# Optimization experiments

Measured on AMD Instinct MI355X. Metric: run time of the kernel, lower is better.

## Reference

```python
import jax, jax.numpy as jnp
import numpy as np

D_MODEL = 768
N_HEADS = 12
D_KEYS = 64
D_LLM = 4096
D_INNER = N_HEADS * D_KEYS  # 768


def setup_inputs() -> dict:
    key = jax.random.key(0)
    ks = jax.random.split(key, 12)
    inp = {
        "target_embedding": jax.random.normal(ks[0], (8, 1024, D_MODEL), dtype=jnp.float32),
        "source_embedding": jax.random.normal(ks[1], (1000, D_LLM), dtype=jnp.float32),
        "value_embedding": jax.random.normal(ks[2], (1000, D_LLM), dtype=jnp.float32),
        # Linear params stored as [in, out] (y = x @ W + b)
        "Wq": jax.random.normal(ks[3], (D_MODEL, D_INNER), dtype=jnp.float32) * 0.02,
        "bq": jnp.zeros((D_INNER,), dtype=jnp.float32),
        "Wk": jax.random.normal(ks[4], (D_LLM, D_INNER), dtype=jnp.float32) * 0.02,
        "bk": jnp.zeros((D_INNER,), dtype=jnp.float32),
        "Wv": jax.random.normal(ks[5], (D_LLM, D_INNER), dtype=jnp.float32) * 0.02,
        "bv": jnp.zeros((D_INNER,), dtype=jnp.float32),
        "Wo": jax.random.normal(ks[6], (D_INNER, D_LLM), dtype=jnp.float32) * 0.02,
        "bo": jnp.zeros((D_LLM,), dtype=jnp.float32),
    }
    return inp


def reference(target_embedding, source_embedding, value_embedding,
              Wq, bq, Wk, bk, Wv, bv, Wo, bo):
    B, L, _ = target_embedding.shape
    S, _ = source_embedding.shape
    H, E = N_HEADS, D_KEYS
    # projections
    q = (target_embedding @ Wq + bq).reshape(B, L, H, E)  # [B,L,H,E]
    k = (source_embedding @ Wk + bk).reshape(S, H, E)     # [S,H,E] broadcast over batch
    v = (value_embedding @ Wv + bv).reshape(S, H, E)      # [S,H,E]
    scale = 1.0 / np.sqrt(E).astype(np.float32)
    scores = jnp.einsum('blhe,she->bhls', q, k) * scale   # [B,H,L,S]
    A = jax.nn.softmax(scores, axis=-1)                   # dropout is identity at eval
    out = jnp.einsum('bhls,she->blhe', A, v).reshape(B, L, H * E)
    return out @ Wo + bo                                  # [B,L,d_llm]
```

## Files before the change

kernel.cpp:

```cpp
#include <hip/hip_runtime.h>
#include <cstdint>
#include <type_traits>


typedef unsigned short u16;
typedef __attribute__((ext_vector_type(8))) short bf16x8;
typedef __attribute__((ext_vector_type(4))) float f32x4;
typedef __attribute__((ext_vector_type(16))) float f32x16;
typedef __attribute__((ext_vector_type(4))) float fvec4;
typedef __attribute__((ext_vector_type(4))) unsigned short u16x4;
typedef __attribute__((ext_vector_type(4))) unsigned int u32x4;
typedef __attribute__((ext_vector_type(2))) unsigned int u32x2;

using gld_src_t = const __attribute__((address_space(1))) void*;
using gld_dst_t = __attribute__((address_space(3))) void*;

static __device__ __forceinline__ u16 bf16_rne(float f) {
  uint32_t u = __builtin_bit_cast(uint32_t, f);
  u += 0x7fffu + ((u >> 16) & 1u);
  return (u16)(u >> 16);
}

static __device__ __forceinline__ float exp2_fast(float x) {
  float r; asm("v_exp_f32 %0, %1" : "=v"(r) : "v"(x)); return r;
}

static __device__ __forceinline__ uint32_t pk_bf16(float a, float b) {
  return (uint32_t)bf16_rne(a) | ((uint32_t)bf16_rne(b) << 16);
}

__global__ void convert_pad_bf16(const float* __restrict__ in, u16* __restrict__ out,
                                 int validR, int C, long n4) {
  long stride = (long)gridDim.x * blockDim.x;
  for (long i = (long)blockIdx.x * blockDim.x + threadIdx.x; i < n4; i += stride) {
    long e = i << 2;
    int r = (int)(e / C);
    u16x4 o;
    if (r < validR) {
      fvec4 v = *(const fvec4*)(in + e);
      o[0] = bf16_rne(v[0]); o[1] = bf16_rne(v[1]);
      o[2] = bf16_rne(v[2]); o[3] = bf16_rne(v[3]);
    } else {
      o[0] = 0; o[1] = 0; o[2] = 0; o[3] = 0;
    }
    *(u16x4*)(out + e) = o;
  }
}

template <bool F32IN>
__global__ void transpose_to_bf16(const void* __restrict__ inv, u16* __restrict__ out,
                                  int R, int C) {
  __shared__ u16 tile[32][33];
  int bc = blockIdx.x * 32, br = blockIdx.y * 32;
  int tx = threadIdx.x & 31, ty = threadIdx.x >> 5;
#pragma unroll
  for (int i = 0; i < 4; ++i) {
    int r = br + ty + i * 8, c = bc + tx;
    u16 bits = 0;
    if (r < R && c < C) {
      if constexpr (F32IN) bits = bf16_rne(((const float*)inv)[(size_t)r * C + c]);
      else                 bits = ((const u16*)inv)[(size_t)r * C + c];
    }
    tile[ty + i * 8][tx] = bits;
  }
  __syncthreads();
#pragma unroll
  for (int i = 0; i < 4; ++i) {
    int orow = bc + ty + i * 8, oc = br + tx;
    if (orow < C && oc < R) out[(size_t)orow * R + oc] = tile[tx][ty + i * 8];
  }
}

template <typename CT>
__global__ __launch_bounds__(256, 2) void gemm_bt_128p(
    const u16* __restrict__ A, const u16* __restrict__ B,
    const float* __restrict__ bias, CT* __restrict__ C,
    int N, int K, float escale) {
  __shared__ u16 As[2][128 * 64];
  __shared__ u16 Bs[2][128 * 64];

  const int tid = threadIdx.x, lane = tid & 63, w = tid >> 6;
  const int lr = lane & 15, lg = lane >> 4;
  const int wr = (w >> 1) * 64, wc = (w & 1) * 64;

  const int nbx = N >> 7;
  const int bid = blockIdx.y * gridDim.x + blockIdx.x;
  const int cpx = (gridDim.x * gridDim.y) >> 3;
  const int swz = (bid & 7) * cpx + (bid >> 3);
  const int bm = (swz / nbx) * 128, bn = (swz % nbx) * 128;

  f32x4 acc[4][4] = {};

  auto STAGE = [&](int t, int buf) {
#pragma unroll
    for (int it = 0; it < 4; ++it) {
      const int s = it * 256 + tid;
      const int r = s >> 3;
      const int cg = (s & 7) ^ (r & 7);
      const int ldsb = (it * 256 + w * 64) * 16;
      __builtin_amdgcn_global_load_lds(
          (gld_src_t)(const void*)(A + (size_t)(bm + r) * K + t * 64 + cg * 8),
          (gld_dst_t)((char*)&As[buf][0] + ldsb), 16, 0, 0);
      __builtin_amdgcn_global_load_lds(
          (gld_src_t)(const void*)(B + (size_t)(bn + r) * K + t * 64 + cg * 8),
          (gld_dst_t)((char*)&Bs[buf][0] + ldsb), 16, 0, 0);
    }
  };

  auto LDF = [&](const u16* base, int R, int CB) {
    return *(const bf16x8*)((const char*)base + (size_t)R * 128 + (CB ^ ((R & 7) << 4)));
  };

  STAGE(0, 0);

  const int nk = K >> 6;
  for (int t = 0; t < nk; ++t) {
    const int cur = t & 1;
    if (t + 1 < nk) {
      STAGE(t + 1, cur ^ 1);
      asm volatile("s_waitcnt vmcnt(8)" ::: "memory");
    } else {
      asm volatile("s_waitcnt vmcnt(0)" ::: "memory");
    }
    __builtin_amdgcn_s_barrier();
    __builtin_amdgcn_sched_barrier(0);

    const u16* as = &As[cur][0];
    const u16* bs = &Bs[cur][0];

    bf16x8 af[4][2], bfr[4][2];
#pragma unroll
    for (int m = 0; m < 4; ++m)
#pragma unroll
      for (int kk = 0; kk < 2; ++kk)
        af[m][kk] = LDF(as, wr + m * 16 + lr, kk * 64 + lg * 16);
#pragma unroll
    for (int n = 0; n < 4; ++n)
#pragma unroll
      for (int kk = 0; kk < 2; ++kk)
        bfr[n][kk] = LDF(bs, wc + n * 16 + lr, kk * 64 + lg * 16);

    __builtin_amdgcn_s_setprio(1);
#pragma unroll
    for (int kk = 0; kk < 2; ++kk)
#pragma unroll
      for (int m = 0; m < 4; ++m)
#pragma unroll
        for (int n = 0; n < 4; ++n)
          acc[m][n] = __builtin_amdgcn_mfma_f32_16x16x32_bf16(
              af[m][kk], bfr[n][kk], acc[m][n], 0, 0, 0);
    __builtin_amdgcn_s_setprio(0);

    __builtin_amdgcn_sched_barrier(0);
    __builtin_amdgcn_s_barrier();
  }

#pragma unroll
  for (int n = 0; n < 4; ++n) {
    const int col = bn + wc + n * 16 + lr;
    const float bv = bias[col];
#pragma unroll
    for (int m = 0; m < 4; ++m) {
      const int row0 = bm + wr + m * 16 + lg * 4;
#pragma unroll
      for (int r = 0; r < 4; ++r) {
        float v = (acc[m][n][r] + bv) * escale;
        if constexpr (std::is_same<CT, u16>::value)
          C[(size_t)(row0 + r) * N + col] = bf16_rne(v);
        else
          C[(size_t)(row0 + r) * N + col] = v;
      }
    }
  }
}

__global__ __launch_bounds__(512, 2) void gemm_bt_256p(
    const u16* __restrict__ A, const u16* __restrict__ B,
    const float* __restrict__ bias, float* __restrict__ C,
    int N, int K) {
  __shared__ u16 As[4][128 * 64];
  __shared__ u16 Bs[4][128 * 64];

  const int tid = threadIdx.x, lane = tid & 63, w = tid >> 6;
  const int lr = lane & 15, lg = lane >> 4;
  const int wr = w >> 2, wcol = w & 3;

  const int nbx = N >> 8;
  const int bid = blockIdx.y * gridDim.x + blockIdx.x;
  const int cpx = (gridDim.x * gridDim.y) >> 3;
  const int swz = (bid & 7) * cpx + (bid >> 3);
  const int bm = (swz / nbx) * 256, bn = (swz % nbx) * 256;

  f32x4 acc[8][4] = {};

  auto STAGE_UNIT = [&](int t, int buf, int mat) {
#pragma unroll
    for (int it = 0; it < 2; ++it) {
      const int s = it * 512 + tid;
      const int rp = s >> 3;
      const int cl = (s & 7) ^ (rp & 7);
      const int gr = (cl >> 2) * 128 + rp;
      const int gc = cl & 3;
      const int ldsb = (it * 512 + w * 64) * 16;
      const u16* src = (mat ? B : A) + (size_t)((mat ? bn : bm) + gr) * K + t * 32 + gc * 8;
      __builtin_amdgcn_global_load_lds((gld_src_t)(const void*)src,
          (gld_dst_t)((char*)(mat ? &Bs[buf][0] : &As[buf][0]) + ldsb), 16, 0, 0);
    }
  };

  auto LDF = [&](const u16* base, int gr, int klg) {
    const int byte = (gr & 127) * 128 + (((((gr >> 7) * 4 + klg) << 4)) ^ ((gr & 7) << 4));
    return *(const bf16x8*)((const char*)base + byte);
  };

  STAGE_UNIT(0, 0, 0); STAGE_UNIT(0, 0, 1);
  STAGE_UNIT(1, 1, 0); STAGE_UNIT(1, 1, 1);
  asm volatile("s_waitcnt vmcnt(4)" ::: "memory");
  __builtin_amdgcn_s_barrier();
  __builtin_amdgcn_sched_barrier(0);

  const int nk = K >> 5;
  bf16x8 bfr[4];
  for (int t = 0; t < nk; ++t) {
    const int cur = t & 3;
    const u16* as = &As[cur][0];
    const u16* bs = &Bs[cur][0];
#pragma unroll
    for (int p = 0; p < 2; ++p) {
      bf16x8 af[4];
#pragma unroll
      for (int m = 0; m < 4; ++m)
        af[m] = LDF(as, wr * 128 + (p * 4 + m) * 16 + lr, lg);
      if (p == 0) {
#pragma unroll
        for (int n = 0; n < 4; ++n)
          bfr[n] = LDF(bs, wcol * 64 + n * 16 + lr, lg);
      }
      if (t + 2 < nk) STAGE_UNIT(t + 2, (t + 2) & 3, p);
      if (p == 1) {
        if (t + 2 < nk)      asm volatile("s_waitcnt vmcnt(4)" ::: "memory");
        else if (t + 1 < nk) asm volatile("s_waitcnt vmcnt(0)" ::: "memory");
      }
      __builtin_amdgcn_s_barrier();
      __builtin_amdgcn_sched_barrier(0);
      __builtin_amdgcn_s_setprio(1);
#pragma unroll
      for (int m = 0; m < 4; ++m)
#pragma unroll
        for (int n = 0; n < 4; ++n)
          acc[p * 4 + m][n] = __builtin_amdgcn_mfma_f32_16x16x32_bf16(
              af[m], bfr[n], acc[p * 4 + m][n], 0, 0, 0);
      __builtin_amdgcn_s_setprio(0);
      __builtin_amdgcn_sched_barrier(0);
    }
  }

  float bv[4];
#pragma unroll
  for (int nf = 0; nf < 4; ++nf) bv[nf] = bias[bn + wcol * 64 + nf * 16 + lr];
#pragma unroll
  for (int mf = 0; mf < 8; ++mf) {
    const int row0 = bm + wr * 128 + mf * 16 + lg * 4;
#pragma unroll
    for (int nf = 0; nf < 4; ++nf) {
      const int col = bn + wcol * 64 + nf * 16 + lr;
#pragma unroll
      for (int r = 0; r < 4; ++r)
        C[(size_t)(row0 + r) * N + col] = acc[mf][nf][r] + bv[nf];
    }
  }
}

__global__ __launch_bounds__(256) void gemm_kv_splitk(
    const u16* __restrict__ Sb, const u16* __restrict__ Vbi,
    const u16* __restrict__ WkT, const u16* __restrict__ WvT,
    float* __restrict__ part) {
  const int z = blockIdx.z;
  const u16* A = (z >> 2) ? Vbi : Sb;
  const u16* B = (z >> 2) ? WvT : WkT;
  float* C = part + (size_t)z * (1024 * 768);
  const int kofs = (z & 3) * 1024;

  __shared__ u16 As[128 * 32];
  __shared__ u16 Bs[128 * 32];
  const int tid = threadIdx.x, w = tid >> 6, lane = tid & 63;
  const int lr = lane & 15, lg = lane >> 4;
  const int bm = blockIdx.y * 128, bn = blockIdx.x * 128;
  const int wr = (w >> 1) * 64, wc = (w & 1) * 64;
  f32x4 acc[4][4] = {};

  for (int kt = 0; kt < 32; ++kt) {
#pragma unroll
    for (int j = 0; j < 2; ++j) {
      int cb = j * 256 + w * 64;
      int c = cb + lane;
      const u16* gA = A + (size_t)(bm + (c >> 2)) * 4096 + kofs + kt * 32 + (c & 3) * 8;
      __builtin_amdgcn_global_load_lds((gld_src_t)(const void*)gA,
                                       (gld_dst_t)(As + (size_t)cb * 8), 16, 0, 0);
      const u16* gB = B + (size_t)(bn + (c >> 2)) * 4096 + kofs + kt * 32 + (c & 3) * 8;
      __builtin_amdgcn_global_load_lds((gld_src_t)(const void*)gB,
                                       (gld_dst_t)(Bs + (size_t)cb * 8), 16, 0, 0);
    }
    __syncthreads();
    bf16x8 af[4], bfr[4];
#pragma unroll
    for (int m = 0; m < 4; ++m)
      af[m] = *(const bf16x8*)(As + (wr + m * 16 + lr) * 32 + lg * 8);
#pragma unroll
    for (int n = 0; n < 4; ++n)
      bfr[n] = *(const bf16x8*)(Bs + (wc + n * 16 + lr) * 32 + lg * 8);
#pragma unroll
    for (int m = 0; m < 4; ++m)
#pragma unroll
      for (int n = 0; n < 4; ++n)
        acc[m][n] = __builtin_amdgcn_mfma_f32_16x16x32_bf16(af[m], bfr[n], acc[m][n], 0, 0, 0);
    __syncthreads();
  }
#pragma unroll
  for (int n = 0; n < 4; ++n) {
    int col = bn + wc + n * 16 + lr;
#pragma unroll
    for (int m = 0; m < 4; ++m) {
      int row0 = bm + wr + m * 16 + lg * 4;
#pragma unroll
      for (int r = 0; r < 4; ++r)
        C[(size_t)(row0 + r) * 768 + col] = acc[m][n][r];
    }
  }
}

__global__ __launch_bounds__(256) void kv_reduce(const float* __restrict__ part,
                                                 const float* __restrict__ bk,
                                                 const float* __restrict__ bv,
                                                 u16* __restrict__ Kp, u16* __restrict__ Vp) {
  const int mat = blockIdx.y;
  const long e = ((long)blockIdx.x * 256 + threadIdx.x) * 4;
  const float* p0 = part + (size_t)mat * 4 * 786432 + e;
  fvec4 s = *(const fvec4*)p0;
  s += *(const fvec4*)(p0 + 786432);
  s += *(const fvec4*)(p0 + 2 * 786432);
  s += *(const fvec4*)(p0 + 3 * 786432);
  const float* bias = mat ? bv : bk;
  int col = (int)(e % 768);
  fvec4 bb = *(const fvec4*)(bias + col);
  s += bb;
  u16x4 o;
  o[0] = bf16_rne(s[0]); o[1] = bf16_rne(s[1]); o[2] = bf16_rne(s[2]); o[3] = bf16_rne(s[3]);
  u16* dst = mat ? Vp : Kp;
  *(u16x4*)(dst + e) = o;
}

__global__ __launch_bounds__(256, 3) void attn_flash(
    const u16* __restrict__ Q,
    const u16* __restrict__ Kb,
    const u16* __restrict__ VT,
    u16* __restrict__ O) {
  constexpr int DM = 768, SPAD = 1024;
  __shared__ u16 Ks[3][64 * 64];
  __shared__ u16 VTs[3][64 * 64];

  const int tid = threadIdx.x, w = tid >> 6, lane = tid & 63;
  const int q5 = lane & 31, hi = lane >> 5, l7 = lane & 7;
  const int h = blockIdx.y;
  const int qrow = blockIdx.x * 128 + w * 32 + q5;

  bf16x8 qf[4];
#pragma unroll
  for (int dstep = 0; dstep < 4; ++dstep)
    qf[dstep] = *(const bf16x8*)(Q + (size_t)qrow * DM + h * 64 + dstep * 16 + hi * 8);

  auto STAGE = [&](int ch, int buf) {
#pragma unroll
    for (int it = 0; it < 2; ++it) {
      int slot = it * 256 + w * 64 + lane;
      int row = slot >> 3;
      int cg = (slot & 7) ^ (row & 7);
      __builtin_amdgcn_global_load_lds(
          (gld_src_t)(const void*)(Kb + (size_t)(ch * 64 + row) * DM + h * 64 + cg * 8),
          (gld_dst_t)(&Ks[buf][(size_t)(it * 256 + w * 64) * 8]), 16, 0, 0);
      __builtin_amdgcn_global_load_lds(
          (gld_src_t)(const void*)(VT + (size_t)(h * 64 + row) * SPAD + ch * 64 + cg * 8),
          (gld_dst_t)(&VTs[buf][(size_t)(it * 256 + w * 64) * 8]), 16, 0, 0);
    }
  };

  STAGE(0, 0);
  STAGE(1, 1);

  float m_run = -3.0e38f, l_part = 0.0f;
  f32x16 oa0 = {}, oa1 = {};

  for (int ch = 0; ch < 16; ++ch) {
    const int cur = ch % 3;
    if (ch < 15) asm volatile("s_waitcnt vmcnt(4)" ::: "memory");
    else         asm volatile("s_waitcnt vmcnt(0)" ::: "memory");
    __builtin_amdgcn_s_barrier();
    __builtin_amdgcn_sched_barrier(0);

    const char* kbase = (const char*)&Ks[cur][0];
    const char* vbase = (const char*)&VTs[cur][0];

    f32x16 sc0 = {}, sc1 = {};
#pragma unroll
    for (int dstep = 0; dstep < 4; ++dstep) {
      const int colb = (dstep * 32 + hi * 16);
      bf16x8 kf0 = *(const bf16x8*)(kbase + (size_t)q5 * 128 + (colb ^ (l7 << 4)));
      bf16x8 kf1 = *(const bf16x8*)(kbase + (size_t)(32 + q5) * 128 + (colb ^ (l7 << 4)));
      sc0 = __builtin_amdgcn_mfma_f32_32x32x16_bf16(kf0, qf[dstep], sc0, 0, 0, 0);
      sc1 = __builtin_amdgcn_mfma_f32_32x32x16_bf16(kf1, qf[dstep], sc1, 0, 0, 0);
    }
    if (ch == 15) {
#pragma unroll
      for (int r = 4; r < 16; ++r) sc1[r] = -3.0e38f;
    }

    float mi = sc0[0];
#pragma unroll
    for (int r = 1; r < 16; ++r) mi = fmaxf(mi, sc0[r]);
#pragma unroll
    for (int r = 0; r < 16; ++r) mi = fmaxf(mi, sc1[r]);
    float cm = fmaxf(mi, __shfl_xor(mi, 32, 64));

    if (__any(cm > m_run + 8.0f)) {
      float mn = fmaxf(m_run, cm);
      float fsc = exp2_fast(m_run - mn);
      m_run = mn;
      l_part *= fsc;
#pragma unroll
      for (int r = 0; r < 16; ++r) { oa0[r] *= fsc; oa1[r] *= fsc; }
    }

#pragma unroll
    for (int r = 0; r < 16; ++r) {
      float p0 = exp2_fast(sc0[r] - m_run); l_part += p0; sc0[r] = p0;
      float p1 = exp2_fast(sc1[r] - m_run); l_part += p1; sc1[r] = p1;
    }

#pragma unroll
    for (int st = 0; st < 2; ++st) {
#pragma unroll
      for (int ks = 0; ks < 2; ++ks) {
        float pv0, pv1, pv2, pv3, pv4, pv5, pv6, pv7;
        if (st == 0) {
          if (ks == 0) { pv0=sc0[0];pv1=sc0[1];pv2=sc0[2];pv3=sc0[3];pv4=sc0[4];pv5=sc0[5];pv6=sc0[6];pv7=sc0[7]; }
          else         { pv0=sc0[8];pv1=sc0[9];pv2=sc0[10];pv3=sc0[11];pv4=sc0[12];pv5=sc0[13];pv6=sc0[14];pv7=sc0[15]; }
        } else {
          if (ks == 0) { pv0=sc1[0];pv1=sc1[1];pv2=sc1[2];pv3=sc1[3];pv4=sc1[4];pv5=sc1[5];pv6=sc1[6];pv7=sc1[7]; }
          else         { pv0=sc1[8];pv1=sc1[9];pv2=sc1[10];pv3=sc1[11];pv4=sc1[12];pv5=sc1[13];pv6=sc1[14];pv7=sc1[15]; }
        }
        uint32_t a = pk_bf16(pv0, pv1), b = pk_bf16(pv2, pv3);
        uint32_t c = pk_bf16(pv4, pv5), d = pk_bf16(pv6, pv7);
        uint32_t sa = (uint32_t)__shfl_xor((int)a, 32, 64);
        uint32_t sb = (uint32_t)__shfl_xor((int)b, 32, 64);
        uint32_t sc_ = (uint32_t)__shfl_xor((int)c, 32, 64);
        uint32_t sd = (uint32_t)__shfl_xor((int)d, 32, 64);
        u32x4 jw;
        jw[0] = hi ? sc_ : a;
        jw[1] = hi ? sd  : b;
        jw[2] = hi ? c   : sa;
        jw[3] = hi ? d   : sb;
        bf16x8 pB = __builtin_bit_cast(bf16x8, jw);
        const int colb = (st * 64 + ks * 32 + hi * 16);
#pragma unroll
        for (int dt = 0; dt < 2; ++dt) {
          bf16x8 vtf = *(const bf16x8*)(vbase + (size_t)(dt * 32 + q5) * 128 + (colb ^ (l7 << 4)));
          if (dt == 0) oa0 = __builtin_amdgcn_mfma_f32_32x32x16_bf16(vtf, pB, oa0, 0, 0, 0);
          else         oa1 = __builtin_amdgcn_mfma_f32_32x32x16_bf16(vtf, pB, oa1, 0, 0, 0);
        }
      }
    }

    if (ch + 2 < 16) STAGE(ch + 2, (ch + 2) % 3);
  }

  float ool = 1.0f / (l_part + __shfl_xor(l_part, 32, 64));
  u16* obase = O + (size_t)qrow * DM + h * 64;
#pragma unroll
  for (int dt = 0; dt < 2; ++dt) {
#pragma unroll
    for (int g = 0; g < 4; ++g) {
      float v0, v1, v2, v3;
      if (dt == 0) { v0 = oa0[4*g]; v1 = oa0[4*g+1]; v2 = oa0[4*g+2]; v3 = oa0[4*g+3]; }
      else         { v0 = oa1[4*g]; v1 = oa1[4*g+1]; v2 = oa1[4*g+2]; v3 = oa1[4*g+3]; }
      u32x2 st2;
      st2[0] = pk_bf16(v0 * ool, v1 * ool);
      st2[1] = pk_bf16(v2 * ool, v3 * ool);
      *(u32x2*)(obase + dt * 32 + g * 8 + hi * 4) = st2;
    }
  }
}

extern "C" void kernel_launch(void* const* d_in, const int* in_sizes, int n_in,
                              void* d_out, int out_size, void* d_ws, size_t ws_size,
                              hipStream_t stream) {
  (void)in_sizes; (void)n_in; (void)out_size; (void)ws_size;
  const float* target = (const float*)d_in[0];
  const float* source = (const float*)d_in[1];
  const float* value  = (const float*)d_in[2];
  const float* Wq = (const float*)d_in[3];
  const float* bq = (const float*)d_in[4];
  const float* Wk = (const float*)d_in[5];
  const float* bk = (const float*)d_in[6];
  const float* Wv = (const float*)d_in[7];
  const float* bv = (const float*)d_in[8];
  const float* Wo = (const float*)d_in[9];
  const float* bo = (const float*)d_in[10];
  float* out = (float*)d_out;

  char* ws = (char*)d_ws;
  size_t off = 0;
  auto carve = [&](size_t bytes) { void* p = ws + off; off += (bytes + 255) & ~(size_t)255; return p; };
  u16* Xb  = (u16*)carve(8192ull * 768 * 2);
  u16* Sb  = (u16*)carve(1024ull * 4096 * 2);
  u16* Vbi = (u16*)carve(1024ull * 4096 * 2);
  u16* WqT = (u16*)carve(768ull * 768 * 2);
  u16* WkT = (u16*)carve(768ull * 4096 * 2);
  u16* WvT = (u16*)carve(768ull * 4096 * 2);
  u16* WoT = (u16*)carve(4096ull * 768 * 2);
  u16* Qb  = (u16*)carve(8192ull * 768 * 2);
  u16* Kp  = (u16*)carve(1024ull * 768 * 2);
  u16* Vp  = (u16*)carve(1024ull * 768 * 2);
  u16* VTp = (u16*)carve(768ull * 1024 * 2);
  u16* Ob  = (u16*)carve(8192ull * 768 * 2);

  const float SCL = 0.18033688011112042f;

  convert_pad_bf16<<<2048, 256, 0, stream>>>(target, Xb, 8192, 768, (8192ll * 768) / 4);
  convert_pad_bf16<<<2048, 256, 0, stream>>>(source, Sb, 1000, 4096, (1024ll * 4096) / 4);
  convert_pad_bf16<<<2048, 256, 0, stream>>>(value,  Vbi, 1000, 4096, (1024ll * 4096) / 4);
  transpose_to_bf16<true><<<dim3(24, 24),  256, 0, stream>>>(Wq, WqT, 768, 768);
  transpose_to_bf16<true><<<dim3(24, 128), 256, 0, stream>>>(Wk, WkT, 4096, 768);
  transpose_to_bf16<true><<<dim3(24, 128), 256, 0, stream>>>(Wv, WvT, 4096, 768);
  transpose_to_bf16<true><<<dim3(128, 24), 256, 0, stream>>>(Wo, WoT, 768, 4096);

  gemm_kv_splitk<<<dim3(6, 8, 8), 256, 0, stream>>>(Sb, Vbi, WkT, WvT, out);
  kv_reduce<<<dim3(768, 2), 256, 0, stream>>>(out, bk, bv, Kp, Vp);
  transpose_to_bf16<false><<<dim3(24, 32), 256, 0, stream>>>(Vp, VTp, 1024, 768);

  gemm_bt_128p<u16><<<dim3(6, 64), 256, 0, stream>>>(Xb, WqT, bq, Qb, 768, 768, SCL);

  attn_flash<<<dim3(64, 12), 256, 0, stream>>>(Qb, Kp, VTp, Ob);

  gemm_bt_256p<<<dim3(16, 32), 512, 0, stream>>>(Ob, WoT, bo, out, 4096, 768);
}
```

Before: 213.7 us.

## Pipeline KV split-K GEMM, fuse V reduce with transpose, merge prep launches

Replaces the single-buffered KV split-K GEMM with a double-buffered version that uses K=64 tiles, an XOR-swizzled LDS layout, async global-to-LDS loads and MFMA priority hints. It also fuses the V partial-sum reduction with the transpose into VT, which drops the intermediate Vp buffer and one launch. The three fp32-to-bf16 conversions become one launch, and the Wk/Wv transposes are merged into another. The aim is to cut launch overhead and memory traffic in the preprocessing chain and to hide load latency in the KV GEMM, at the cost of more LDS per block.

```diff
diff --git a/kernel.cpp b/kernel.cpp
--- a/kernel.cpp
+++ b/kernel.cpp
@@ -29,8 +29,16 @@
   return (uint32_t)bf16_rne(a) | ((uint32_t)bf16_rne(b) << 16);
 }
 
-__global__ void convert_pad_bf16(const float* __restrict__ in, u16* __restrict__ out,
-                                 int validR, int C, long n4) {
+__global__ void convert_all_bf16(const float* __restrict__ t0, u16* __restrict__ o0,
+                                 const float* __restrict__ t1, u16* __restrict__ o1,
+                                 const float* __restrict__ t2, u16* __restrict__ o2) {
+  const int sel = blockIdx.y;
+  const float* in = sel == 0 ? t0 : (sel == 1 ? t1 : t2);
+  u16* out = sel == 0 ? o0 : (sel == 1 ? o1 : o2);
+  const int C = sel == 0 ? 768 : 4096;
+  const int validR = sel == 0 ? 8192 : 1000;
+  const long n4 = sel == 0 ? (8192ll * 768 / 4) : (1024ll * 4096 / 4);
+
   long stride = (long)gridDim.x * blockDim.x;
   for (long i = (long)blockIdx.x * blockDim.x + threadIdx.x; i < n4; i += stride) {
     long e = i << 2;
@@ -47,9 +55,11 @@
   }
 }
 
-template <bool F32IN>
-__global__ void transpose_to_bf16(const void* __restrict__ inv, u16* __restrict__ out,
-                                  int R, int C) {
+__global__ void transpose_to_bf16_f32(const float* __restrict__ in0, u16* __restrict__ out0,
+                                      const float* __restrict__ in1, u16* __restrict__ out1,
+                                      int R, int C) {
+  const float* inv = blockIdx.z ? in1 : in0;
+  u16* out = blockIdx.z ? out1 : out0;
   __shared__ u16 tile[32][33];
   int bc = blockIdx.x * 32, br = blockIdx.y * 32;
   int tx = threadIdx.x & 31, ty = threadIdx.x >> 5;
@@ -57,10 +67,7 @@
   for (int i = 0; i < 4; ++i) {
     int r = br + ty + i * 8, c = bc + tx;
     u16 bits = 0;
-    if (r < R && c < C) {
-      if constexpr (F32IN) bits = bf16_rne(((const float*)inv)[(size_t)r * C + c]);
-      else                 bits = ((const u16*)inv)[(size_t)r * C + c];
-    }
+    if (r < R && c < C) bits = bf16_rne(inv[(size_t)r * C + c]);
     tile[ty + i * 8][tx] = bits;
   }
   __syncthreads();
@@ -174,6 +181,143 @@
   }
 }
 
+__global__ __launch_bounds__(256, 2) void gemm_kv_splitk_p(
+    const u16* __restrict__ Sb, const u16* __restrict__ Vbi,
+    const u16* __restrict__ WkT, const u16* __restrict__ WvT,
+    float* __restrict__ part) {
+  const int z = blockIdx.z;
+  const u16* A = (z >> 2) ? Vbi : Sb;
+  const u16* B = (z >> 2) ? WvT : WkT;
+  float* C = part + (size_t)z * (1024 * 768);
+  const int kofs = (z & 3) * 1024;
+  constexpr int K = 4096;
+
+  __shared__ u16 As[2][128 * 64];
+  __shared__ u16 Bs[2][128 * 64];
+
+  const int tid = threadIdx.x, lane = tid & 63, w = tid >> 6;
+  const int lr = lane & 15, lg = lane >> 4;
+  const int wr = (w >> 1) * 64, wc = (w & 1) * 64;
+  const int bm = blockIdx.y * 128, bn = blockIdx.x * 128;
+
+  f32x4 acc[4][4] = {};
+
+  auto STAGE = [&](int t, int buf) {
+#pragma unroll
+    for (int it = 0; it < 4; ++it) {
+      const int s = it * 256 + tid;
+      const int r = s >> 3;
+      const int cg = (s & 7) ^ (r & 7);
+      const int ldsb = (it * 256 + w * 64) * 16;
+      __builtin_amdgcn_global_load_lds(
+          (gld_src_t)(const void*)(A + (size_t)(bm + r) * K + kofs + t * 64 + cg * 8),
+          (gld_dst_t)((char*)&As[buf][0] + ldsb), 16, 0, 0);
+      __builtin_amdgcn_global_load_lds(
+          (gld_src_t)(const void*)(B + (size_t)(bn + r) * K + kofs + t * 64 + cg * 8),
+          (gld_dst_t)((char*)&Bs[buf][0] + ldsb), 16, 0, 0);
+    }
+  };
+
+  auto LDF = [&](const u16* base, int R, int CB) {
+    return *(const bf16x8*)((const char*)base + (size_t)R * 128 + (CB ^ ((R & 7) << 4)));
+  };
+
+  STAGE(0, 0);
+
+  for (int t = 0; t < 16; ++t) {
+    const int cur = t & 1;
+    if (t + 1 < 16) {
+      STAGE(t + 1, cur ^ 1);
+      asm volatile("s_waitcnt vmcnt(8)" ::: "memory");
+    } else {
+      asm volatile("s_waitcnt vmcnt(0)" ::: "memory");
+    }
+    __builtin_amdgcn_s_barrier();
+    __builtin_amdgcn_sched_barrier(0);
+
+    const u16* as = &As[cur][0];
+    const u16* bs = &Bs[cur][0];
+
+    bf16x8 af[4][2], bfr[4][2];
+#pragma unroll
+    for (int m = 0; m < 4; ++m)
+#pragma unroll
+      for (int kk = 0; kk < 2; ++kk)
+        af[m][kk] = LDF(as, wr + m * 16 + lr, kk * 64 + lg * 16);
+#pragma unroll
+    for (int n = 0; n < 4; ++n)
+#pragma unroll
+      for (int kk = 0; kk < 2; ++kk)
+        bfr[n][kk] = LDF(bs, wc + n * 16 + lr, kk * 64 + lg * 16);
+
+    __builtin_amdgcn_s_setprio(1);
+#pragma unroll
+    for (int kk = 0; kk < 2; ++kk)
+#pragma unroll
+      for (int m = 0; m < 4; ++m)
+#pragma unroll
+        for (int n = 0; n < 4; ++n)
+          acc[m][n] = __builtin_amdgcn_mfma_f32_16x16x32_bf16(
+              af[m][kk], bfr[n][kk], acc[m][n], 0, 0, 0);
+    __builtin_amdgcn_s_setprio(0);
+
+    __builtin_amdgcn_sched_barrier(0);
+    __builtin_amdgcn_s_barrier();
+  }
+
+#pragma unroll
+  for (int n = 0; n < 4; ++n) {
+    const int col = bn + wc + n * 16 + lr;
+#pragma unroll
+    for (int m = 0; m < 4; ++m) {
+      const int row0 = bm + wr + m * 16 + lg * 4;
+#pragma unroll
+      for (int r = 0; r < 4; ++r)
+        C[(size_t)(row0 + r) * 768 + col] = acc[m][n][r];
+    }
+  }
+}
+
+__global__ __launch_bounds__(256) void kv_reduce_k(const float* __restrict__ part,
+                                                   const float* __restrict__ bk,
+                                                   u16* __restrict__ Kp) {
+  const long e = ((long)blockIdx.x * 256 + threadIdx.x) * 4;
+  const float* p0 = part + e;
+  fvec4 s = *(const fvec4*)p0;
+  s += *(const fvec4*)(p0 + 786432);
+  s += *(const fvec4*)(p0 + 2 * 786432);
+  s += *(const fvec4*)(p0 + 3 * 786432);
+  int col = (int)(e % 768);
+  s += *(const fvec4*)(bk + col);
+  u16x4 o;
+  o[0] = bf16_rne(s[0]); o[1] = bf16_rne(s[1]); o[2] = bf16_rne(s[2]); o[3] = bf16_rne(s[3]);
+  *(u16x4*)(Kp + e) = o;
+}
+
+__global__ __launch_bounds__(256) void kv_reduce_vt(const float* __restrict__ part,
+                                                    const float* __restrict__ bv,
+                                                    u16* __restrict__ VTp) {
+  __shared__ u16 tile[32][33];
+  const float* pv = part + 4ull * 786432;
+  const int c0 = blockIdx.x * 32, r0 = blockIdx.y * 32;
+  const int tx = threadIdx.x & 31, ty = threadIdx.x >> 5;
+#pragma unroll
+  for (int i = 0; i < 4; ++i) {
+    const int r = r0 + ty + i * 8, c = c0 + tx;
+    const size_t idx = (size_t)r * 768 + c;
+    float s = pv[idx] + pv[idx + 786432] + pv[idx + 2 * 786432] + pv[idx + 3 * 786432]
+            + bv[c];
+    tile[ty + i * 8][tx] = bf16_rne(s);
+  }
+  __syncthreads();
+#pragma unroll
+  for (int i = 0; i < 4; ++i) {
+    const int vr = c0 + ty + i * 8;
+    const int vc = r0 + tx;
+    VTp[(size_t)vr * 1024 + vc] = tile[tx][ty + i * 8];
+  }
+}
+
 __global__ __launch_bounds__(512, 2) void gemm_bt_256p(
     const u16* __restrict__ A, const u16* __restrict__ B,
     const float* __restrict__ bias, float* __restrict__ C,
@@ -269,85 +413,6 @@
         C[(size_t)(row0 + r) * N + col] = acc[mf][nf][r] + bv[nf];
     }
   }
-}
-
-__global__ __launch_bounds__(256) void gemm_kv_splitk(
-    const u16* __restrict__ Sb, const u16* __restrict__ Vbi,
-    const u16* __restrict__ WkT, const u16* __restrict__ WvT,
-    float* __restrict__ part) {
-  const int z = blockIdx.z;
-  const u16* A = (z >> 2) ? Vbi : Sb;
-  const u16* B = (z >> 2) ? WvT : WkT;
-  float* C = part + (size_t)z * (1024 * 768);
-  const int kofs = (z & 3) * 1024;
-
-  __shared__ u16 As[128 * 32];
-  __shared__ u16 Bs[128 * 32];
-  const int tid = threadIdx.x, w = tid >> 6, lane = tid & 63;
-  const int lr = lane & 15, lg = lane >> 4;
-  const int bm = blockIdx.y * 128, bn = blockIdx.x * 128;
-  const int wr = (w >> 1) * 64, wc = (w & 1) * 64;
-  f32x4 acc[4][4] = {};
-
-  for (int kt = 0; kt < 32; ++kt) {
-#pragma unroll
-    for (int j = 0; j < 2; ++j) {
-      int cb = j * 256 + w * 64;
-      int c = cb + lane;
-      const u16* gA = A + (size_t)(bm + (c >> 2)) * 4096 + kofs + kt * 32 + (c & 3) * 8;
-      __builtin_amdgcn_global_load_lds((gld_src_t)(const void*)gA,
-                                       (gld_dst_t)(As + (size_t)cb * 8), 16, 0, 0);
-      const u16* gB = B + (size_t)(bn + (c >> 2)) * 4096 + kofs + kt * 32 + (c & 3) * 8;
-      __builtin_amdgcn_global_load_lds((gld_src_t)(const void*)gB,
-                                       (gld_dst_t)(Bs + (size_t)cb * 8), 16, 0, 0);
-    }
-    __syncthreads();
-    bf16x8 af[4], bfr[4];
-#pragma unroll
-    for (int m = 0; m < 4; ++m)
-      af[m] = *(const bf16x8*)(As + (wr + m * 16 + lr) * 32 + lg * 8);
-#pragma unroll
-    for (int n = 0; n < 4; ++n)
-      bfr[n] = *(const bf16x8*)(Bs + (wc + n * 16 + lr) * 32 + lg * 8);
-#pragma unroll
-    for (int m = 0; m < 4; ++m)
-#pragma unroll
-      for (int n = 0; n < 4; ++n)
-        acc[m][n] = __builtin_amdgcn_mfma_f32_16x16x32_bf16(af[m], bfr[n], acc[m][n], 0, 0, 0);
-    __syncthreads();
-  }
-#pragma unroll
-  for (int n = 0; n < 4; ++n) {
-    int col = bn + wc + n * 16 + lr;
-#pragma unroll
-    for (int m = 0; m < 4; ++m) {
-      int row0 = bm + wr + m * 16 + lg * 4;
-#pragma unroll
-      for (int r = 0; r < 4; ++r)
-        C[(size_t)(row0 + r) * 768 + col] = acc[m][n][r];
-    }
-  }
-}
-
-__global__ __launch_bounds__(256) void kv_reduce(const float* __restrict__ part,
-                                                 const float* __restrict__ bk,
-                                                 const float* __restrict__ bv,
-                                                 u16* __restrict__ Kp, u16* __restrict__ Vp) {
-  const int mat = blockIdx.y;
-  const long e = ((long)blockIdx.x * 256 + threadIdx.x) * 4;
-  const float* p0 = part + (size_t)mat * 4 * 786432 + e;
-  fvec4 s = *(const fvec4*)p0;
-  s += *(const fvec4*)(p0 + 786432);
-  s += *(const fvec4*)(p0 + 2 * 786432);
-  s += *(const fvec4*)(p0 + 3 * 786432);
-  const float* bias = mat ? bv : bk;
-  int col = (int)(e % 768);
-  fvec4 bb = *(const fvec4*)(bias + col);
-  s += bb;
-  u16x4 o;
-  o[0] = bf16_rne(s[0]); o[1] = bf16_rne(s[1]); o[2] = bf16_rne(s[2]); o[3] = bf16_rne(s[3]);
-  u16* dst = mat ? Vp : Kp;
-  *(u16x4*)(dst + e) = o;
 }
 
 __global__ __launch_bounds__(256, 3) void attn_flash(
@@ -519,23 +584,19 @@
   u16* WoT = (u16*)carve(4096ull * 768 * 2);
   u16* Qb  = (u16*)carve(8192ull * 768 * 2);
   u16* Kp  = (u16*)carve(1024ull * 768 * 2);
-  u16* Vp  = (u16*)carve(1024ull * 768 * 2);
   u16* VTp = (u16*)carve(768ull * 1024 * 2);
   u16* Ob  = (u16*)carve(8192ull * 768 * 2);
 
   const float SCL = 0.18033688011112042f;
 
-  convert_pad_bf16<<<2048, 256, 0, stream>>>(target, Xb, 8192, 768, (8192ll * 768) / 4);
-  convert_pad_bf16<<<2048, 256, 0, stream>>>(source, Sb, 1000, 4096, (1024ll * 4096) / 4);
-  convert_pad_bf16<<<2048, 256, 0, stream>>>(value,  Vbi, 1000, 4096, (1024ll * 4096) / 4);
-  transpose_to_bf16<true><<<dim3(24, 24),  256, 0, stream>>>(Wq, WqT, 768, 768);
-  transpose_to_bf16<true><<<dim3(24, 128), 256, 0, stream>>>(Wk, WkT, 4096, 768);
-  transpose_to_bf16<true><<<dim3(24, 128), 256, 0, stream>>>(Wv, WvT, 4096, 768);
-  transpose_to_bf16<true><<<dim3(128, 24), 256, 0, stream>>>(Wo, WoT, 768, 4096);
-
-  gemm_kv_splitk<<<dim3(6, 8, 8), 256, 0, stream>>>(Sb, Vbi, WkT, WvT, out);
-  kv_reduce<<<dim3(768, 2), 256, 0, stream>>>(out, bk, bv, Kp, Vp);
-  transpose_to_bf16<false><<<dim3(24, 32), 256, 0, stream>>>(Vp, VTp, 1024, 768);
+  convert_all_bf16<<<dim3(1024, 3), 256, 0, stream>>>(target, Xb, source, Sb, value, Vbi);
+  transpose_to_bf16_f32<<<dim3(24, 24, 1),  256, 0, stream>>>(Wq, WqT, Wq, WqT, 768, 768);
+  transpose_to_bf16_f32<<<dim3(24, 128, 2), 256, 0, stream>>>(Wk, WkT, Wv, WvT, 4096, 768);
+  transpose_to_bf16_f32<<<dim3(128, 24, 1), 256, 0, stream>>>(Wo, WoT, Wo, WoT, 768, 4096);
+
+  gemm_kv_splitk_p<<<dim3(6, 8, 8), 256, 0, stream>>>(Sb, Vbi, WkT, WvT, out);
+  kv_reduce_k<<<768, 256, 0, stream>>>(out, bk, Kp);
+  kv_reduce_vt<<<dim3(24, 32), 256, 0, stream>>>(out, bv, VTp);
 
   gemm_bt_128p<u16><<<dim3(6, 64), 256, 0, stream>>>(Xb, WqT, bq, Qb, 768, 768, SCL);
 
```

New measurement: 200.7 us. 1.06x faster.
